# Kernel tuning notes

Measured on AMD Instinct MI355X. Metric: run time of the kernel, lower is better.

## Reference

```python
import jax, jax.numpy as jnp
import numpy as np


def setup_inputs() -> dict:
    key = jax.random.key(0)
    k1, k2, k3 = jax.random.split(key, 3)
    N, E, C = 100000, 3200000, 256
    x = jax.random.normal(k1, (N, C), dtype=jnp.float32)
    edge_index = jax.random.randint(k2, (2, E), 0, N, dtype=jnp.int64)
    W = jax.random.normal(k3, (C, 1), dtype=jnp.float32) / np.sqrt(C)
    b = jnp.zeros((1,), dtype=jnp.float32)
    return {"x": x, "edge_index": edge_index, "W": W, "b": b}


def reference(x, edge_index, W, b):
    # GCNConv(in_channels, 1) with default add_self_loops=True, symmetric norm,
    # followed by Softplus.
    N = x.shape[0]
    loop = jnp.arange(N, dtype=edge_index.dtype)
    src = jnp.concatenate([edge_index[0], loop])  # [E+N]
    dst = jnp.concatenate([edge_index[1], loop])  # [E+N]
    # degree on target index (unit edge weights, self-loops included)
    deg = jax.ops.segment_sum(jnp.ones_like(dst, dtype=x.dtype), dst, num_segments=N)
    dinv = jnp.where(deg > 0, jax.lax.rsqrt(deg), 0.0)
    norm = dinv[src] * dinv[dst]  # [E+N]
    h = x @ W  # [N, 1] linear transform before aggregation (no bias)
    msg = norm[:, None] * h[src]  # [E+N, 1]
    out = jax.ops.segment_sum(msg, dst, num_segments=N) + b  # [N, 1]
    return jax.nn.softplus(out)
```

## Files before the change

kernel.cpp:

```cpp
#include <hip/hip_runtime.h>
#include <cmath>
#include <cstdint>


#define NBSHIFT 8
#define NLOCAL  (1 << NBSHIFT)
#define KPART   1024
#define SRCBITS 17

__global__ __launch_bounds__(256) void k_dot(const float* __restrict__ x,
                                             const float* __restrict__ W,
                                             float* __restrict__ h, int N) {
    int tid  = blockIdx.x * blockDim.x + threadIdx.x;
    int lane = threadIdx.x & 63;
    int nw   = (gridDim.x * blockDim.x) >> 6;
    const float4 wv = *reinterpret_cast<const float4*>(W + lane * 4);
    for (int row = tid >> 6; row < N; row += nw) {
        const float4 xv = *reinterpret_cast<const float4*>(x + (size_t)row * 256 + lane * 4);
        float s = xv.x * wv.x + xv.y * wv.y + xv.z * wv.z + xv.w * wv.w;
        #pragma unroll
        for (int o = 32; o >= 1; o >>= 1) s += __shfl_xor(s, o, 64);
        if (lane == 0) h[row] = s;
    }
}

__global__ __launch_bounds__(256) void k_count(const int* __restrict__ dst,
                                               unsigned* __restrict__ countsT,
                                               int E, int NB, int CH) {
    __shared__ unsigned cnt[512];
    for (int j = threadIdx.x; j < 512; j += 256) cnt[j] = 0;
    __syncthreads();
    int s = blockIdx.x * CH, e = min(E, s + CH);
    int e4 = s + (((e - s) >> 2) << 2);
    for (int i = s + (int)threadIdx.x * 4; i < e4; i += 1024) {
        int4 v = *reinterpret_cast<const int4*>(dst + i);
        atomicAdd(&cnt[((unsigned)v.x) >> NBSHIFT], 1u);
        atomicAdd(&cnt[((unsigned)v.y) >> NBSHIFT], 1u);
        atomicAdd(&cnt[((unsigned)v.z) >> NBSHIFT], 1u);
        atomicAdd(&cnt[((unsigned)v.w) >> NBSHIFT], 1u);
    }
    for (int i = e4 + threadIdx.x; i < e; i += 256)
        atomicAdd(&cnt[((unsigned)dst[i]) >> NBSHIFT], 1u);
    __syncthreads();
    for (int j = threadIdx.x; j < NB; j += 256)
        countsT[(size_t)j * KPART + blockIdx.x] = cnt[j];
}

__global__ __launch_bounds__(256) void k_scanA(const unsigned* __restrict__ countsT,
                                               unsigned* __restrict__ bucketTot) {
    __shared__ unsigned red[256];
    int j = blockIdx.x, t = threadIdx.x;
    uint4 c = *reinterpret_cast<const uint4*>(countsT + (size_t)j * KPART + t * 4);
    red[t] = c.x + c.y + c.z + c.w;
    __syncthreads();
    for (int s = 128; s > 0; s >>= 1) {
        if (t < s) red[t] += red[t + s];
        __syncthreads();
    }
    if (t == 0) bucketTot[j] = red[0];
}

__global__ __launch_bounds__(512) void k_scanB(const unsigned* __restrict__ bucketTot,
                                               unsigned* __restrict__ bucketBase,
                                               int NB) {
    __shared__ unsigned arr[512];
    int t = threadIdx.x;
    unsigned own = (t < NB) ? bucketTot[t] : 0u;
    arr[t] = own;
    __syncthreads();
    for (int off = 1; off < 512; off <<= 1) {
        unsigned add = (t >= off) ? arr[t - off] : 0u;
        __syncthreads();
        arr[t] += add;
        __syncthreads();
    }
    if (t < NB) bucketBase[t] = arr[t] - own;
    if (t == NB - 1) bucketBase[NB] = arr[t];
}

__global__ __launch_bounds__(256) void k_scanC(const unsigned* __restrict__ countsT,
                                               const unsigned* __restrict__ bucketBase,
                                               unsigned* __restrict__ baseT) {
    __shared__ unsigned arr[256];
    int j = blockIdx.x, t = threadIdx.x;
    uint4 c = *reinterpret_cast<const uint4*>(countsT + (size_t)j * KPART + t * 4);
    unsigned own = c.x + c.y + c.z + c.w;
    arr[t] = own;
    __syncthreads();
    for (int off = 1; off < 256; off <<= 1) {
        unsigned add = (t >= off) ? arr[t - off] : 0u;
        __syncthreads();
        arr[t] += add;
        __syncthreads();
    }
    unsigned base = bucketBase[j] + (arr[t] - own);
    uint4 o;
    o.x = base;
    o.y = base + c.x;
    o.z = base + c.x + c.y;
    o.w = base + c.x + c.y + c.z;
    *reinterpret_cast<uint4*>(baseT + (size_t)j * KPART + t * 4) = o;
}

__global__ __launch_bounds__(256) void k_part(const int* __restrict__ src,
                                              const int* __restrict__ dst,
                                              const unsigned* __restrict__ baseT,
                                              unsigned* __restrict__ sorted,
                                              int E, int NB, int CH) {
    __shared__ unsigned base[512];
    __shared__ unsigned rank[512];
    for (int j = threadIdx.x; j < NB; j += 256) {
        base[j] = baseT[(size_t)j * KPART + blockIdx.x];
        rank[j] = 0;
    }
    __syncthreads();
    int s = blockIdx.x * CH, e = min(E, s + CH);
    int e4 = s + (((e - s) >> 2) << 2);
    for (int i = s + (int)threadIdx.x * 4; i < e4; i += 1024) {
        int4 dv = *reinterpret_cast<const int4*>(dst + i);
        int4 sv = *reinterpret_cast<const int4*>(src + i);
        unsigned d, j, r;
        d = (unsigned)dv.x; j = d >> NBSHIFT; r = atomicAdd(&rank[j], 1u);
        sorted[base[j] + r] = ((d & (NLOCAL - 1u)) << SRCBITS) | (unsigned)sv.x;
        d = (unsigned)dv.y; j = d >> NBSHIFT; r = atomicAdd(&rank[j], 1u);
        sorted[base[j] + r] = ((d & (NLOCAL - 1u)) << SRCBITS) | (unsigned)sv.y;
        d = (unsigned)dv.z; j = d >> NBSHIFT; r = atomicAdd(&rank[j], 1u);
        sorted[base[j] + r] = ((d & (NLOCAL - 1u)) << SRCBITS) | (unsigned)sv.z;
        d = (unsigned)dv.w; j = d >> NBSHIFT; r = atomicAdd(&rank[j], 1u);
        sorted[base[j] + r] = ((d & (NLOCAL - 1u)) << SRCBITS) | (unsigned)sv.w;
    }
    for (int i = e4 + threadIdx.x; i < e; i += 256) {
        unsigned d = (unsigned)dst[i];
        unsigned j = d >> NBSHIFT;
        unsigned r = atomicAdd(&rank[j], 1u);
        sorted[base[j] + r] = ((d & (NLOCAL - 1u)) << SRCBITS) | (unsigned)src[i];
    }
}

__global__ __launch_bounds__(512) void k_deg(const unsigned* __restrict__ sorted,
                                             const unsigned* __restrict__ bucketBase,
                                             const float* __restrict__ h,
                                             float* __restrict__ dinv,
                                             float* __restrict__ g,
                                             int N) {
    __shared__ unsigned acc[NLOCAL];
    int j = blockIdx.x, t = threadIdx.x;
    if (t < NLOCAL) acc[t] = 0;
    __syncthreads();
    unsigned s0 = bucketBase[j], e0 = bucketBase[j + 1];
    for (unsigned i = s0 + t; i < e0; i += 512)
        atomicAdd(&acc[sorted[i] >> SRCBITS], 1u);
    __syncthreads();
    if (t < NLOCAL) {
        int n = (j << NBSHIFT) + t;
        if (n < N) {
            float di = rsqrtf((float)(acc[t] + 1u));
            dinv[n] = di;
            g[n]    = di * h[n];
        }
    }
}

__global__ __launch_bounds__(512) void k_agg(const unsigned* __restrict__ sorted,
                                             const unsigned* __restrict__ bucketBase,
                                             const float* __restrict__ g,
                                             const float* __restrict__ dinv,
                                             const float* __restrict__ b,
                                             float* __restrict__ out,
                                             int N) {
    __shared__ float acc[NLOCAL];
    int j = blockIdx.x, t = threadIdx.x;
    if (t < NLOCAL) acc[t] = 0.0f;
    __syncthreads();
    unsigned s0 = bucketBase[j], e0 = bucketBase[j + 1];
    for (unsigned i = s0 + t; i < e0; i += 512) {
        unsigned p = sorted[i];
        atomicAdd(&acc[p >> SRCBITS], g[p & ((1u << SRCBITS) - 1u)]);
    }
    __syncthreads();
    if (t < NLOCAL) {
        int n = (j << NBSHIFT) + t;
        if (n < N) {
            float v = dinv[n] * (acc[t] + g[n]) + b[0];
            out[n] = fmaxf(v, 0.0f) + log1pf(expf(-fabsf(v)));
        }
    }
}

extern "C" void kernel_launch(void* const* d_in, const int* in_sizes, int n_in,
                              void* d_out, int out_size, void* d_ws, size_t ws_size,
                              hipStream_t stream) {
    const float* x  = (const float*)d_in[0];
    const int*   ei = (const int*)d_in[1];
    const float* W  = (const float*)d_in[2];
    const float* b  = (const float*)d_in[3];
    float* out = (float*)d_out;

    int N = in_sizes[0] / 256;
    int E = in_sizes[1] / 2;
    const int* src = ei;
    const int* dst = ei + E;

    int NB = (N + NLOCAL - 1) >> NBSHIFT;
    int CH = (((E + KPART - 1) / KPART) + 3) & ~3;

    float*    h       = (float*)d_ws;
    float*    dinv    = h + N;
    float*    g       = dinv + N;
    unsigned* sorted  = (unsigned*)(g + N);
    unsigned* countsT = sorted + E;
    unsigned* baseT   = countsT + (size_t)NB * KPART;
    unsigned* btot    = baseT + (size_t)NB * KPART;
    unsigned* bbase   = btot + NB;

    k_dot  <<<2048, 256, 0, stream>>>(x, W, h, N);
    k_count<<<KPART, 256, 0, stream>>>(dst, countsT, E, NB, CH);
    k_scanA<<<NB, 256, 0, stream>>>(countsT, btot);
    k_scanB<<<1, 512, 0, stream>>>(btot, bbase, NB);
    k_scanC<<<NB, 256, 0, stream>>>(countsT, bbase, baseT);
    k_part <<<KPART, 256, 0, stream>>>(src, dst, baseT, sorted, E, NB, CH);
    k_deg  <<<NB, 512, 0, stream>>>(sorted, bbase, h, dinv, g, N);
    k_agg  <<<NB, 512, 0, stream>>>(sorted, bbase, g, dinv, b, out, N);
}
```

Before: 248.8 us.

## Fuse dot with count, fold bucket-base scan into scanC, widen agg blocks

Merges the x·W row-dot kernel into the destination-bucket count kernel, so one launch of KPART blocks does both. The single-block exclusive scan over bucket totals is removed: each scanC block now reduces the totals of all preceding buckets itself and writes its own bucket base. The deg and agg kernels move to 1024-thread blocks and compute bucket end from base plus total. This removes two launches and their serialization gaps. In exchange, the dot product now runs on 1024 blocks instead of 2048, and every scanC block re-reads and reduces up to 512 bucket totals.

```diff
diff --git a/kernel.cpp b/kernel.cpp
--- a/kernel.cpp
+++ b/kernel.cpp
@@ -8,9 +8,12 @@
 #define KPART   1024
 #define SRCBITS 17
 
-__global__ __launch_bounds__(256) void k_dot(const float* __restrict__ x,
-                                             const float* __restrict__ W,
-                                             float* __restrict__ h, int N) {
+__global__ __launch_bounds__(256) void k_front(const float* __restrict__ x,
+                                               const float* __restrict__ W,
+                                               const int* __restrict__ dst,
+                                               float* __restrict__ h,
+                                               unsigned* __restrict__ countsT,
+                                               int N, int E, int NB, int CH) {
     int tid  = blockIdx.x * blockDim.x + threadIdx.x;
     int lane = threadIdx.x & 63;
     int nw   = (gridDim.x * blockDim.x) >> 6;
@@ -22,11 +25,7 @@
         for (int o = 32; o >= 1; o >>= 1) s += __shfl_xor(s, o, 64);
         if (lane == 0) h[row] = s;
     }
-}
-
-__global__ __launch_bounds__(256) void k_count(const int* __restrict__ dst,
-                                               unsigned* __restrict__ countsT,
-                                               int E, int NB, int CH) {
+
     __shared__ unsigned cnt[512];
     for (int j = threadIdx.x; j < 512; j += 256) cnt[j] = 0;
     __syncthreads();
@@ -47,7 +46,7 @@
 }
 
 __global__ __launch_bounds__(256) void k_scanA(const unsigned* __restrict__ countsT,
-                                               unsigned* __restrict__ bucketTot) {
+                                               unsigned* __restrict__ btot) {
     __shared__ unsigned red[256];
     int j = blockIdx.x, t = threadIdx.x;
     uint4 c = *reinterpret_cast<const uint4*>(countsT + (size_t)j * KPART + t * 4);
@@ -57,32 +56,30 @@
         if (t < s) red[t] += red[t + s];
         __syncthreads();
     }
-    if (t == 0) bucketTot[j] = red[0];
-}
-
-__global__ __launch_bounds__(512) void k_scanB(const unsigned* __restrict__ bucketTot,
-                                               unsigned* __restrict__ bucketBase,
+    if (t == 0) btot[j] = red[0];
+}
+
+__global__ __launch_bounds__(256) void k_scanC(const unsigned* __restrict__ countsT,
+                                               const unsigned* __restrict__ btot,
+                                               unsigned* __restrict__ bbase,
+                                               unsigned* __restrict__ baseT,
                                                int NB) {
-    __shared__ unsigned arr[512];
-    int t = threadIdx.x;
-    unsigned own = (t < NB) ? bucketTot[t] : 0u;
-    arr[t] = own;
-    __syncthreads();
-    for (int off = 1; off < 512; off <<= 1) {
-        unsigned add = (t >= off) ? arr[t - off] : 0u;
-        __syncthreads();
-        arr[t] += add;
-        __syncthreads();
-    }
-    if (t < NB) bucketBase[t] = arr[t] - own;
-    if (t == NB - 1) bucketBase[NB] = arr[t];
-}
-
-__global__ __launch_bounds__(256) void k_scanC(const unsigned* __restrict__ countsT,
-                                               const unsigned* __restrict__ bucketBase,
-                                               unsigned* __restrict__ baseT) {
+    __shared__ unsigned red[256];
     __shared__ unsigned arr[256];
-    int j = blockIdx.x, t = threadIdx.x;
+    __shared__ unsigned sBase;
+    int j = blockIdx.x, t = threadIdx.x;
+
+    unsigned v = 0;
+    if (t < j) v += btot[t];
+    if (t + 256 < j) v += btot[t + 256];
+    red[t] = v;
+    __syncthreads();
+    for (int s = 128; s > 0; s >>= 1) {
+        if (t < s) red[t] += red[t + s];
+        __syncthreads();
+    }
+    if (t == 0) { sBase = red[0]; bbase[j] = red[0]; }
+
     uint4 c = *reinterpret_cast<const uint4*>(countsT + (size_t)j * KPART + t * 4);
     unsigned own = c.x + c.y + c.z + c.w;
     arr[t] = own;
@@ -93,7 +90,7 @@
         arr[t] += add;
         __syncthreads();
     }
-    unsigned base = bucketBase[j] + (arr[t] - own);
+    unsigned base = sBase + (arr[t] - own);
     uint4 o;
     o.x = base;
     o.y = base + c.x;
@@ -137,18 +134,19 @@
     }
 }
 
-__global__ __launch_bounds__(512) void k_deg(const unsigned* __restrict__ sorted,
-                                             const unsigned* __restrict__ bucketBase,
-                                             const float* __restrict__ h,
-                                             float* __restrict__ dinv,
-                                             float* __restrict__ g,
-                                             int N) {
+__global__ __launch_bounds__(1024) void k_deg(const unsigned* __restrict__ sorted,
+                                              const unsigned* __restrict__ bbase,
+                                              const unsigned* __restrict__ btot,
+                                              const float* __restrict__ h,
+                                              float* __restrict__ dinv,
+                                              float* __restrict__ g,
+                                              int N) {
     __shared__ unsigned acc[NLOCAL];
     int j = blockIdx.x, t = threadIdx.x;
     if (t < NLOCAL) acc[t] = 0;
     __syncthreads();
-    unsigned s0 = bucketBase[j], e0 = bucketBase[j + 1];
-    for (unsigned i = s0 + t; i < e0; i += 512)
+    unsigned s0 = bbase[j], e0 = s0 + btot[j];
+    for (unsigned i = s0 + t; i < e0; i += 1024)
         atomicAdd(&acc[sorted[i] >> SRCBITS], 1u);
     __syncthreads();
     if (t < NLOCAL) {
@@ -161,19 +159,20 @@
     }
 }
 
-__global__ __launch_bounds__(512) void k_agg(const unsigned* __restrict__ sorted,
-                                             const unsigned* __restrict__ bucketBase,
-                                             const float* __restrict__ g,
-                                             const float* __restrict__ dinv,
-                                             const float* __restrict__ b,
-                                             float* __restrict__ out,
-                                             int N) {
+__global__ __launch_bounds__(1024) void k_agg(const unsigned* __restrict__ sorted,
+                                              const unsigned* __restrict__ bbase,
+                                              const unsigned* __restrict__ btot,
+                                              const float* __restrict__ g,
+                                              const float* __restrict__ dinv,
+                                              const float* __restrict__ b,
+                                              float* __restrict__ out,
+                                              int N) {
     __shared__ float acc[NLOCAL];
     int j = blockIdx.x, t = threadIdx.x;
     if (t < NLOCAL) acc[t] = 0.0f;
     __syncthreads();
-    unsigned s0 = bucketBase[j], e0 = bucketBase[j + 1];
-    for (unsigned i = s0 + t; i < e0; i += 512) {
+    unsigned s0 = bbase[j], e0 = s0 + btot[j];
+    for (unsigned i = s0 + t; i < e0; i += 1024) {
         unsigned p = sorted[i];
         atomicAdd(&acc[p >> SRCBITS], g[p & ((1u << SRCBITS) - 1u)]);
     }
@@ -213,12 +212,10 @@
     unsigned* btot    = baseT + (size_t)NB * KPART;
     unsigned* bbase   = btot + NB;
 
-    k_dot  <<<2048, 256, 0, stream>>>(x, W, h, N);
-    k_count<<<KPART, 256, 0, stream>>>(dst, countsT, E, NB, CH);
+    k_front<<<KPART, 256, 0, stream>>>(x, W, dst, h, countsT, N, E, NB, CH);
     k_scanA<<<NB, 256, 0, stream>>>(countsT, btot);
-    k_scanB<<<1, 512, 0, stream>>>(btot, bbase, NB);
-    k_scanC<<<NB, 256, 0, stream>>>(countsT, bbase, baseT);
+    k_scanC<<<NB, 256, 0, stream>>>(countsT, btot, bbase, baseT, NB);
     k_part <<<KPART, 256, 0, stream>>>(src, dst, baseT, sorted, E, NB, CH);
-    k_deg  <<<NB, 512, 0, stream>>>(sorted, bbase, h, dinv, g, N);
-    k_agg  <<<NB, 512, 0, stream>>>(sorted, bbase, g, dinv, b, out, N);
-}
+    k_deg  <<<NB, 1024, 0, stream>>>(sorted, bbase, btot, h, dinv, g, N);
+    k_agg  <<<NB, 1024, 0, stream>>>(sorted, bbase, btot, g, dinv, b, out, N);
+}
```

Result: faster. 238.3 us (-4.2%).
